# Kernel optimization log

Measured on AMD Instinct MI355X. Metric: run time of the kernel, lower is better.

The kernel has to match this reference:

```python
import jax, jax.numpy as jnp
import numpy as np

T = 2_000_000  # timesteps


def setup_inputs() -> dict:
    key = jax.random.key(0)
    u = jax.random.normal(key, (T, 2), dtype=jnp.float32) * 10.0  # external forces per step
    x0 = jnp.zeros((4,), dtype=jnp.float32)  # [z1, v1, z2, v2]
    c = jnp.array([10.0, 10.0, 10.0], dtype=jnp.float32)   # trainable damping c1,c2,c3
    m = jnp.array([20.0, 10.0], dtype=jnp.float32)          # masses m1,m2 (frozen)
    k = jnp.array([2.0e3, 1.0e3, 5.0e3], dtype=jnp.float32) # stiffness k1,k2,k3 (frozen)
    dt = jnp.float32(0.002)
    return {"u": u, "x0": x0, "c": c, "m": m, "k": k, "dt": dt}


def reference(u, x0, c, m, k, dt):
    c1, c2, c3 = c[0], c[1], c[2]
    m1, m2 = m[0], m[1]
    k1, k2, k3 = k[0], k[1], k[2]

    def deriv(x, ut):
        # x = [z1, v1, z2, v2]; returns dx/dt = [v1, a1, v2, a2]
        z1, v1, z2, v2 = x[0], x[1], x[2], x[3]
        a1 = (ut[0] - (c1 + c2) * v1 + c2 * v2 - (k1 + k2) * z1 + k2 * z2) / m1
        a2 = (ut[1] - (c3 + c2) * v2 + c2 * v1 - (k3 + k2) * z2 + k2 * z1) / m2
        return jnp.stack([v1, a1, v2, a2])

    half = dt * 0.5

    def step(x, ut):
        s1 = deriv(x, ut)
        s2 = deriv(x + half * s1, ut)
        s3 = deriv(x + half * s2, ut)
        s4 = deriv(x + dt * s3, ut)
        xn = x + (dt / 6.0) * (s1 + 2.0 * s2 + 2.0 * s3 + s4)
        y = jnp.stack([xn[0], xn[2]])  # positions z1, z2 (matches cell output)
        return xn, y

    _, ys = jax.lax.scan(step, x0, u)
    return ys  # [T, 2]
```

## Files before the change

kernel.cpp:

```cpp
#include <hip/hip_runtime.h>

#define BLK 256
#define LS  16
#define SPB (BLK*LS)
#define STR (LS+1)

#define WC_M   0
#define WC_N   16
#define WC_SK  24
#define WC_GK  152
#define WC_TOT 296

#define WS_BAR_F32   2048
#define BAR_ARR_U32  0
#define BAR_FLAG_U32 544
#define BAR_BYTES    2304

typedef unsigned long long u64t;
union F2U { float2 f; u64t u; };

#define STEP4(Mx,Nx, s0,s1,s2,s3, ux,uy, n0,n1,n2,n3)                                              \
  n0 = fmaf(Mx[0],s0,  fmaf(Mx[1],s1,  fmaf(Mx[2],s2,  fmaf(Mx[3],s3,  fmaf(Nx[0],ux, Nx[1]*uy))))); \
  n1 = fmaf(Mx[4],s0,  fmaf(Mx[5],s1,  fmaf(Mx[6],s2,  fmaf(Mx[7],s3,  fmaf(Nx[2],ux, Nx[3]*uy))))); \
  n2 = fmaf(Mx[8],s0,  fmaf(Mx[9],s1,  fmaf(Mx[10],s2, fmaf(Mx[11],s3, fmaf(Nx[4],ux, Nx[5]*uy))))); \
  n3 = fmaf(Mx[12],s0, fmaf(Mx[13],s1, fmaf(Mx[14],s2, fmaf(Mx[15],s3, fmaf(Nx[6],ux, Nx[7]*uy)))));

__device__ __forceinline__ float4 aff_apply(const float* Mx, float4 l, float4 c) {
  float4 r;
  r.x = fmaf(Mx[0],l.x,  fmaf(Mx[1],l.y,  fmaf(Mx[2],l.z,  fmaf(Mx[3],l.w,  c.x))));
  r.y = fmaf(Mx[4],l.x,  fmaf(Mx[5],l.y,  fmaf(Mx[6],l.z,  fmaf(Mx[7],l.w,  c.y))));
  r.z = fmaf(Mx[8],l.x,  fmaf(Mx[9],l.y,  fmaf(Mx[10],l.z, fmaf(Mx[11],l.w, c.z))));
  r.w = fmaf(Mx[12],l.x, fmaf(Mx[13],l.y, fmaf(Mx[14],l.z, fmaf(Mx[15],l.w, c.w))));
  return r;
}

__device__ __forceinline__ float4 matvec(const float* Mx, float4 v) {
  return aff_apply(Mx, v, make_float4(0.f, 0.f, 0.f, 0.f));
}

__device__ __forceinline__ float4 shfl_up4(float4 v, int d) {
  return make_float4(__shfl_up(v.x, d, 64), __shfl_up(v.y, d, 64),
                     __shfl_up(v.z, d, 64), __shfl_up(v.w, d, 64));
}

__device__ __forceinline__ double mm_el(double x, double y, int i, int j) {
  double s = 0.0;
  #pragma unroll
  for (int l = 0; l < 4; ++l)
    s = fma(__shfl(x, 4*i + l, 64), __shfl(y, 4*l + j, 64), s);
  return s;
}

__device__ __forceinline__ void wave_setup(const float* __restrict__ cin,
                                           const float* __restrict__ min_,
                                           const float* __restrict__ kin,
                                           const float* __restrict__ dtin,
                                           float* C, int lane) {
  double c1 = cin[0], c2 = cin[1], c3 = cin[2];
  double m1 = min_[0], m2 = min_[1];
  double k1 = kin[0], k2 = kin[1], k3 = kin[2];
  double h  = dtin[0];
  const int i = (lane >> 2) & 3, j = lane & 3;

  double a;
  if (i == 0)      a = (j == 1) ? 1.0 : 0.0;
  else if (i == 2) a = (j == 3) ? 1.0 : 0.0;
  else if (i == 1) a = (j==0) ? -(k1+k2)/m1 : (j==1) ? -(c1+c2)/m1
                     : (j==2) ?  k2/m1      :  c2/m1;
  else             a = (j==0) ?  k2/m2      : (j==1) ?  c2/m2
                     : (j==2) ? -(k3+k2)/m2 : -(c3+c2)/m2;

  const double id = (i == j) ? 1.0 : 0.0;
  double q  = id + (h/4.0)*a;
  double t  = mm_el(a, q,  i, j);
  double r  = id + (h/3.0)*t;
  t         = mm_el(a, r,  i, j);
  double s_ = id + (h/2.0)*t;
  t         = mm_el(a, s_, i, j);
  double m  = id + h*t;
  if (lane < 16) C[WC_M + lane] = (float)m;

  {
    int e = lane & 7, ii = e >> 1, jp = e & 1, col = jp ? 3 : 1;
    double sv = __shfl(s_, 4*ii + col, 64);
    double nv = h * sv / (jp ? m2 : m1);
    if (lane < 8) C[WC_N + lane] = (float)nv;
  }

  double p = m;
  #pragma unroll
  for (int rr = 0; rr < 4; ++rr) p = mm_el(p, p, i, j);
  if (lane < 16) C[WC_SK + lane] = (float)p;
  #pragma unroll
  for (int k = 1; k < 8; ++k) {
    p = mm_el(p, p, i, j);
    if (lane < 16) C[WC_SK + 16*k + lane] = (float)p;
  }
  p = mm_el(p, p, i, j);
  if (lane < 16) C[WC_GK + lane] = (float)p;
  #pragma unroll
  for (int k = 1; k < 9; ++k) {
    p = mm_el(p, p, i, j);
    if (lane < 16) C[WC_GK + 16*k + lane] = (float)p;
  }
}

__device__ __forceinline__ float4 wave_scan(const float* SK, float4 b, int lane) {
  float4 cur = b;
  #pragma unroll
  for (int k = 0; k < 6; ++k) {
    int off = 1 << k;
    float4 l  = shfl_up4(cur, off);
    float4 nv = aff_apply(&SK[16*k], l, cur);
    if (lane >= off) cur = nv;
  }
  return cur;
}

__device__ __forceinline__ float4 cross_wave_excl(const float* SK, const float4* Wagg, int w) {
  float4 E = make_float4(0.f, 0.f, 0.f, 0.f);
  if (w > 0) {
    E = Wagg[0];
    for (int q = 1; q < w; ++q) E = aff_apply(&SK[16*6], E, Wagg[q]);
  }
  return E;
}

__launch_bounds__(BLK, 2)
__global__ void k_fused(const float4* __restrict__ u4,
                        const float* __restrict__ cc, const float* __restrict__ mmp,
                        const float* __restrict__ kp, const float* __restrict__ dtp,
                        float4* __restrict__ agg, unsigned* __restrict__ bar,
                        const float* __restrict__ x0in, float4* __restrict__ out4,
                        int T2, int nblk) {
  __shared__ float  uxp[BLK*STR];
  __shared__ float  uyp[BLK*STR];
  __shared__ float4 MA[512];
  __shared__ float4 MB[512];
  __shared__ float  C[WC_TOT];
  __shared__ float4 Wagg[4];
  const int tid   = threadIdx.x;
  const int bid   = blockIdx.x;
  const int lane  = tid & 63, w = tid >> 6;
  const int base2 = bid * SPB;

  if (tid < 64) wave_setup(cc, mmp, kp, dtp, C, tid);

  #pragma unroll
  for (int kk = 0; kk < SPB/2/BLK; ++kk) {
    int idx4 = tid + kk*BLK;
    int s0 = 2*idx4;
    float4 v = make_float4(0.f, 0.f, 0.f, 0.f);
    if (base2 + s0 < T2) v = u4[(base2 >> 1) + idx4];
    int t0 = s0 >> 4, j0 = s0 & 15;
    int t1 = (s0+1) >> 4, j1 = (s0+1) & 15;
    uxp[t0*STR + j0] = v.x;  uyp[t0*STR + j0] = v.y;
    uxp[t1*STR + j1] = v.z;  uyp[t1*STR + j1] = v.w;
  }
  __syncthreads();

  float Mm[16], Nn[8];
  #pragma unroll
  for (int i = 0; i < 16; ++i) Mm[i] = C[WC_M+i];
  #pragma unroll
  for (int i = 0; i < 8;  ++i) Nn[i] = C[WC_N+i];
  const float* SK = &C[WC_SK];
  const float* GK = &C[WC_GK];

  float b0 = 0.f, b1 = 0.f, b2 = 0.f, b3 = 0.f;
  #pragma unroll
  for (int j = 0; j < LS; ++j) {
    float ux = uxp[tid*STR + j], uy = uyp[tid*STR + j];
    float n0, n1, n2, n3;
    STEP4(Mm, Nn, b0, b1, b2, b3, ux, uy, n0, n1, n2, n3);
    b0 = n0; b1 = n1; b2 = n2; b3 = n3;
  }

  float4 incl = wave_scan(SK, make_float4(b0, b1, b2, b3), lane);
  if (lane == 63) Wagg[w] = incl;
  __syncthreads();

  if (tid == BLK-1) {
    float4 E = cross_wave_excl(SK, Wagg, 3);
    float4 t_ = matvec(&SK[16*6], E);
    F2U lo, hi;
    lo.f = make_float2(incl.x + t_.x, incl.y + t_.y);
    hi.f = make_float2(incl.z + t_.z, incl.w + t_.w);
    u64t* aggu = (u64t*)(agg + bid);
    __hip_atomic_store(aggu + 0, lo.u, __ATOMIC_RELAXED, __HIP_MEMORY_SCOPE_AGENT);
    __hip_atomic_store(aggu + 1, hi.u, __ATOMIC_RELAXED, __HIP_MEMORY_SCOPE_AGENT);
    asm volatile("s_waitcnt vmcnt(0)" ::: "memory");
    __hip_atomic_store(&bar[BAR_ARR_U32 + bid], 1u,
                       __ATOMIC_RELAXED, __HIP_MEMORY_SCOPE_AGENT);
  }

  if (bid == 0 && w == 3) {
    for (;;) {
      int ok = 1;
      #pragma unroll
      for (int it = 0; it < 8; ++it) {
        int i = lane + 64*it;
        unsigned v = __hip_atomic_load(&bar[BAR_ARR_U32 + i],
                                       __ATOMIC_RELAXED, __HIP_MEMORY_SCOPE_AGENT);
        ok &= (i >= nblk) | (v != 0u);
      }
      if (__all(ok)) break;
      __builtin_amdgcn_s_sleep(4);
    }
    if (lane == 63)
      __hip_atomic_store(&bar[BAR_FLAG_U32], 1u,
                         __ATOMIC_RELAXED, __HIP_MEMORY_SCOPE_AGENT);
  } else if (tid == BLK-1) {
    while (!__hip_atomic_load(&bar[BAR_FLAG_U32],
                              __ATOMIC_RELAXED, __HIP_MEMORY_SCOPE_AGENT))
      __builtin_amdgcn_s_sleep(8);
  }
  __syncthreads();

  const int n = nblk + 1;
  #pragma unroll
  for (int j = 0; j < 2; ++j) {
    int i = tid + BLK*j;
    if (i < n) MA[i] = (i == 0) ? make_float4(x0in[0], x0in[1], x0in[2], x0in[3])
                                : agg[i-1];
  }
  __syncthreads();

  float4* Aa = MA; float4* Bb = MB;
  for (int k = 0; k < 9; ++k) {
    int off = 1 << k;
    if (off >= n) break;
    #pragma unroll
    for (int j = 0; j < 2; ++j) {
      int i = tid + BLK*j;
      if (i < n) {
        float4 v = Aa[i];
        if (i >= off) v = aff_apply(&GK[16*k], Aa[i-off], v);
        Bb[i] = v;
      }
    }
    __syncthreads();
    float4* t = Aa; Aa = Bb; Bb = t;
  }

  float4 Xbs = Aa[bid];

  float4 E  = cross_wave_excl(SK, Wagg, w);
  float4 Xw = Xbs;
  if (w & 1) Xw = matvec(&SK[16*6], Xw);
  if (w & 2) Xw = matvec(&SK[16*7], Xw);
  Xw = make_float4(Xw.x + E.x, Xw.y + E.y, Xw.z + E.z, Xw.w + E.w);

  float4 ex = shfl_up4(incl, 1);
  if (lane == 0) ex = make_float4(0.f, 0.f, 0.f, 0.f);
  float4 v = Xw;
  #pragma unroll
  for (int k = 0; k < 6; ++k)
    if (lane & (1 << k)) v = matvec(&SK[16*k], v);
  float x0 = v.x + ex.x, x1 = v.y + ex.y, x2 = v.z + ex.z, x3 = v.w + ex.w;

  #pragma unroll
  for (int j = 0; j < LS; ++j) {
    float ux = uxp[tid*STR + j], uy = uyp[tid*STR + j];
    float n0, n1, n2, n3;
    STEP4(Mm, Nn, x0, x1, x2, x3, ux, uy, n0, n1, n2, n3);
    x0 = n0; x1 = n1; x2 = n2; x3 = n3;
    uxp[tid*STR + j] = x0;
    uyp[tid*STR + j] = x2;
  }
  __syncthreads();

  #pragma unroll
  for (int kk = 0; kk < SPB/2/BLK; ++kk) {
    int idx4 = tid + kk*BLK;
    int s0 = 2*idx4;
    if (base2 + s0 < T2) {
      int t0 = s0 >> 4, j0 = s0 & 15;
      int t1 = (s0+1) >> 4, j1 = (s0+1) & 15;
      out4[(base2 >> 1) + idx4] = make_float4(uxp[t0*STR + j0], uyp[t0*STR + j0],
                                              uxp[t1*STR + j1], uyp[t1*STR + j1]);
    }
  }
}

extern "C" void kernel_launch(void* const* d_in, const int* in_sizes, int n_in,
                              void* d_out, int out_size, void* d_ws, size_t ws_size,
                              hipStream_t stream) {
  const float4* u4  = (const float4*)d_in[0];
  const float*  x0  = (const float*)d_in[1];
  const float*  cc  = (const float*)d_in[2];
  const float*  mm  = (const float*)d_in[3];
  const float*  kk  = (const float*)d_in[4];
  const float*  dt  = (const float*)d_in[5];

  int T2   = in_sizes[0] / 2;
  int nblk = (T2 + SPB - 1) / SPB;

  float*    ws  = (float*)d_ws;
  float4*   agg = (float4*)ws;
  unsigned* bar = (unsigned*)(ws + WS_BAR_F32);

  hipMemsetAsync((void*)bar, 0, BAR_BYTES, stream);

  k_fused<<<nblk, BLK, 0, stream>>>(u4, cc, mm, kk, dt, agg, bar, x0,
                                    (float4*)d_out, T2, nblk);
}
```

Baseline: 94.93 us.

## Double per-thread chunk to 32 steps, halving block count and scan depth

Raises the number of timesteps each thread processes serially from 16 to 32, which halves the number of blocks (about 245 instead of about 489). The block-level carry scan now fits in one element per thread with one fewer doubling level, and the transition-matrix power tables shift by one squaring. The input load is restructured to issue 8 float4 loads before scattering them into shared memory, adding memory-level parallelism. The trade-off is a doubled serial dependency chain per thread, plus higher LDS use and fewer blocks, which lowers occupancy and parallelism on a GPU with many CUs.

Result: no change. 93.08 us (-1.9%).

```diff
diff --git a/kernel.cpp b/kernel.cpp
--- a/kernel.cpp
+++ b/kernel.cpp
@@ -1,7 +1,7 @@
 #include <hip/hip_runtime.h>
 
 #define BLK 256
-#define LS  16
+#define LS  32
 #define SPB (BLK*LS)
 #define STR (LS+1)
 
@@ -9,12 +9,12 @@
 #define WC_N   16
 #define WC_SK  24
 #define WC_GK  152
-#define WC_TOT 296
-
-#define WS_BAR_F32   2048
+#define WC_TOT 280
+
+#define WS_BAR_F32   1024
 #define BAR_ARR_U32  0
-#define BAR_FLAG_U32 544
-#define BAR_BYTES    2304
+#define BAR_FLAG_U32 272
+#define BAR_BYTES    1152
 
 typedef unsigned long long u64t;
 union F2U { float2 f; u64t u; };
@@ -89,7 +89,7 @@
 
   double p = m;
   #pragma unroll
-  for (int rr = 0; rr < 4; ++rr) p = mm_el(p, p, i, j);
+  for (int rr = 0; rr < 5; ++rr) p = mm_el(p, p, i, j);
   if (lane < 16) C[WC_SK + lane] = (float)p;
   #pragma unroll
   for (int k = 1; k < 8; ++k) {
@@ -99,7 +99,7 @@
   p = mm_el(p, p, i, j);
   if (lane < 16) C[WC_GK + lane] = (float)p;
   #pragma unroll
-  for (int k = 1; k < 9; ++k) {
+  for (int k = 1; k < 8; ++k) {
     p = mm_el(p, p, i, j);
     if (lane < 16) C[WC_GK + 16*k + lane] = (float)p;
   }
@@ -135,8 +135,8 @@
                         int T2, int nblk) {
   __shared__ float  uxp[BLK*STR];
   __shared__ float  uyp[BLK*STR];
-  __shared__ float4 MA[512];
-  __shared__ float4 MB[512];
+  __shared__ float4 MA[256];
+  __shared__ float4 MB[256];
   __shared__ float  C[WC_TOT];
   __shared__ float4 Wagg[4];
   const int tid   = threadIdx.x;
@@ -147,15 +147,24 @@
   if (tid < 64) wave_setup(cc, mmp, kp, dtp, C, tid);
 
   #pragma unroll
-  for (int kk = 0; kk < SPB/2/BLK; ++kk) {
-    int idx4 = tid + kk*BLK;
-    int s0 = 2*idx4;
-    float4 v = make_float4(0.f, 0.f, 0.f, 0.f);
-    if (base2 + s0 < T2) v = u4[(base2 >> 1) + idx4];
-    int t0 = s0 >> 4, j0 = s0 & 15;
-    int t1 = (s0+1) >> 4, j1 = (s0+1) & 15;
-    uxp[t0*STR + j0] = v.x;  uyp[t0*STR + j0] = v.y;
-    uxp[t1*STR + j1] = v.z;  uyp[t1*STR + j1] = v.w;
+  for (int b = 0; b < 2; ++b) {
+    float4 vbuf[8];
+    #pragma unroll
+    for (int q = 0; q < 8; ++q) {
+      int idx4 = tid + (b*8 + q)*BLK;
+      float4 v = make_float4(0.f, 0.f, 0.f, 0.f);
+      if (base2 + 2*idx4 < T2) v = u4[(base2 >> 1) + idx4];
+      vbuf[q] = v;
+    }
+    #pragma unroll
+    for (int q = 0; q < 8; ++q) {
+      int idx4 = tid + (b*8 + q)*BLK;
+      int s0 = 2*idx4;
+      int t0 = s0 >> 5, j0 = s0 & 31;
+      int j1 = j0 + 1;
+      uxp[t0*STR + j0] = vbuf[q].x;  uyp[t0*STR + j0] = vbuf[q].y;
+      uxp[t0*STR + j1] = vbuf[q].z;  uyp[t0*STR + j1] = vbuf[q].w;
+    }
   }
   __syncthreads();
 
@@ -198,7 +207,7 @@
     for (;;) {
       int ok = 1;
       #pragma unroll
-      for (int it = 0; it < 8; ++it) {
+      for (int it = 0; it < 4; ++it) {
         int i = lane + 64*it;
         unsigned v = __hip_atomic_load(&bar[BAR_ARR_U32 + i],
                                        __ATOMIC_RELAXED, __HIP_MEMORY_SCOPE_AGENT);
@@ -218,26 +227,18 @@
   __syncthreads();
 
   const int n = nblk + 1;
-  #pragma unroll
-  for (int j = 0; j < 2; ++j) {
-    int i = tid + BLK*j;
-    if (i < n) MA[i] = (i == 0) ? make_float4(x0in[0], x0in[1], x0in[2], x0in[3])
-                                : agg[i-1];
-  }
+  if (tid < n) MA[tid] = (tid == 0) ? make_float4(x0in[0], x0in[1], x0in[2], x0in[3])
+                                    : agg[tid-1];
   __syncthreads();
 
   float4* Aa = MA; float4* Bb = MB;
-  for (int k = 0; k < 9; ++k) {
+  for (int k = 0; k < 8; ++k) {
     int off = 1 << k;
     if (off >= n) break;
-    #pragma unroll
-    for (int j = 0; j < 2; ++j) {
-      int i = tid + BLK*j;
-      if (i < n) {
-        float4 v = Aa[i];
-        if (i >= off) v = aff_apply(&GK[16*k], Aa[i-off], v);
-        Bb[i] = v;
-      }
+    if (tid < n) {
+      float4 v = Aa[tid];
+      if (tid >= off) v = aff_apply(&GK[16*k], Aa[tid-off], v);
+      Bb[tid] = v;
     }
     __syncthreads();
     float4* t = Aa; Aa = Bb; Bb = t;
@@ -275,10 +276,10 @@
     int idx4 = tid + kk*BLK;
     int s0 = 2*idx4;
     if (base2 + s0 < T2) {
-      int t0 = s0 >> 4, j0 = s0 & 15;
-      int t1 = (s0+1) >> 4, j1 = (s0+1) & 15;
+      int t0 = s0 >> 5, j0 = s0 & 31;
+      int j1 = j0 + 1;
       out4[(base2 >> 1) + idx4] = make_float4(uxp[t0*STR + j0], uyp[t0*STR + j0],
-                                              uxp[t1*STR + j1], uyp[t1*STR + j1]);
+                                              uxp[t0*STR + j1], uyp[t0*STR + j1]);
     }
   }
 }
```
